# Optimization experiments

Hardware: AMD Instinct MI355X
Metric: run time of the kernel (lower is better)

The kernel has to match this reference:

```python
import jax, jax.numpy as jnp
import numpy as np

N = 16384   # total queries (= total keys here)
B = 16      # scenes
K = 1024    # keys per scene (key_batch_cnt entries)
L = 32      # local neighborhood size
D = 256     # d_model
H = 8       # nhead
DFF = 1024
LN_EPS = 1e-5


def setup_inputs() -> dict:
    key = jax.random.key(0)
    ks = jax.random.split(key, 32)
    f32 = jnp.float32

    def lin(k, o, i):
        return jax.random.normal(k, (o, i), f32) * 0.02

    idx = jax.random.randint(ks[3], (N, L), 0, K)
    invalid = jax.random.uniform(ks[4], (N, L)) < 0.1
    index_pair = jnp.where(invalid, -1, idx).astype(jnp.int32)

    inp = {
        "tgt": jax.random.normal(ks[0], (N, D), f32),
        "memory": jax.random.normal(ks[1], (N, D), f32),
        "memory_pos_emb": jax.random.normal(ks[2], (N, D), f32),
        "key_batch_cnt": jnp.full((B,), K, dtype=jnp.int32),
        "index_pair": index_pair,
        "index_pair_batch": jnp.repeat(jnp.arange(B, dtype=jnp.int32), K),
        "Wq": lin(ks[5], D, D), "bq": jnp.zeros((D,), f32),
        "Wkc": lin(ks[6], D, D), "bkc": jnp.zeros((D,), f32),
        "Wkp": lin(ks[7], D, D), "bkp": jnp.zeros((D,), f32),
        "Wv": lin(ks[8], D, D), "bv": jnp.zeros((D,), f32),
        "Wo": lin(ks[9], D, D), "bo": jnp.zeros((D,), f32),
        "W1": lin(ks[10], DFF, D), "b1": jnp.zeros((DFF,), f32),
        "W2": lin(ks[11], D, DFF), "b2": jnp.zeros((D,), f32),
        "g2": jnp.ones((D,), f32), "be2": jnp.zeros((D,), f32),
        "g3": jnp.ones((D,), f32), "be3": jnp.zeros((D,), f32),
    }
    return inp


def _ln(x, g, b):
    m = jnp.mean(x, axis=-1, keepdims=True)
    v = jnp.mean((x - m) ** 2, axis=-1, keepdims=True)
    return (x - m) * jax.lax.rsqrt(v + LN_EPS) * g + b


def reference(tgt, memory, memory_pos_emb, key_batch_cnt, index_pair,
              index_pair_batch, Wq, bq, Wkc, bkc, Wkp, bkp, Wv, bv,
              Wo, bo, W1, b1, W2, b2, g2, be2, g3, be3):
    Dh = D // H
    scale = Dh ** -0.5

    # dense projections
    q = tgt @ Wq.T + bq                              # [N, D]
    k = (memory @ Wkc.T + bkc) + (memory_pos_emb @ Wkp.T + bkp)  # content + pos
    v = memory @ Wv.T + bv

    # local-index gather: per-batch indices -> global key indices
    offsets = jnp.concatenate([jnp.zeros((1,), jnp.int32),
                               jnp.cumsum(key_batch_cnt)[:-1].astype(jnp.int32)])
    mask = index_pair < 0                            # [N, L] padded neighbors
    gidx = jnp.where(mask, 0, index_pair + offsets[index_pair_batch][:, None])

    kg = k[gidx].reshape(N, L, H, Dh)                # gathered keys  [N,L,H,Dh]
    vg = v[gidx].reshape(N, L, H, Dh)                # gathered values
    qh = q.reshape(N, H, Dh)

    attn = jnp.einsum('nhd,nlhd->nhl', qh, kg) * scale
    attn = jnp.where(mask[:, None, :], -1e9, attn)
    attn = jax.nn.softmax(attn, axis=-1)
    out = jnp.einsum('nhl,nlhd->nhd', attn, vg).reshape(N, D)
    tgt2 = out @ Wo.T + bo                           # attention out_proj

    x = _ln(tgt + tgt2, g2, be2)
    ff = jax.nn.relu(x @ W1.T + b1) @ W2.T + b2
    return _ln(x + ff, g3, be3)
```

## Files before the change

kernel.cpp:

```cpp
#include <hip/hip_runtime.h>
#include <stdint.h>

#define N_TOT 16384
#define LNEI  32
#define DM    256
#define NH    8
#define DH    32
#define DFF   1024

typedef __attribute__((ext_vector_type(8))) short  short8;
typedef __attribute__((ext_vector_type(4))) float  floatx4;
typedef __attribute__((ext_vector_type(4))) unsigned short ushort4_t;
typedef __attribute__((ext_vector_type(4))) unsigned int uint4_t;

static __device__ __forceinline__ float b2f(unsigned short u) {
  union { unsigned int u; float f; } x; x.u = ((unsigned int)u) << 16; return x.f;
}
static __device__ __forceinline__ unsigned short f2b(float f) {
  union { float f; unsigned int u; } x; x.f = f;
  unsigned int r = x.u + 0x7fffu + ((x.u >> 16) & 1u);
  return (unsigned short)(r >> 16);
}
static __device__ __forceinline__ float lo16(unsigned int d) {
  union { unsigned int u; float f; } x; x.u = d << 16; return x.f;
}
static __device__ __forceinline__ float hi16(unsigned int d) {
  union { unsigned int u; float f; } x; x.u = d & 0xffff0000u; return x.f;
}

#define NSEG 11
struct Seg { const float* src; unsigned short* dst; int cols; int ostride; int ooff; int begin; };
struct SegTable { Seg s[NSEG]; int total; };

__global__ __launch_bounds__(256) void cvt_all(SegTable T, float* biaskv,
                                               const float* bkc, const float* bkp,
                                               const float* bv) {
  int e = (blockIdx.x * 256 + threadIdx.x) * 4;
  if (e >= T.total) {
    int c = e - T.total;
    #pragma unroll
    for (int j = 0; j < 4; ++j, ++c)
      if (c < 512) biaskv[c] = (c < 256) ? (bkc[c] + bkp[c]) : bv[c - 256];
    return;
  }
  int si = 0;
  #pragma unroll
  for (int i = 1; i < NSEG; ++i) if (e >= T.s[i].begin) si = i;
  const Seg s = T.s[si];
  const int le = e - s.begin;
  const int row = le / s.cols;
  const int col = le - row * s.cols;
  floatx4 v = {0.f, 0.f, 0.f, 0.f};
  if (s.src) v = *(const floatx4*)(s.src + le);
  ushort4_t o;
  o.x = f2b(v[0]); o.y = f2b(v[1]); o.z = f2b(v[2]); o.w = f2b(v[3]);
  *(ushort4_t*)(s.dst + (size_t)row * s.ostride + s.ooff + col) = o;
}

static __device__ __forceinline__ void gl_lds16(const unsigned short* g, unsigned short* l) {
  __builtin_amdgcn_global_load_lds(
      (const __attribute__((address_space(1))) unsigned int*)g,
      (__attribute__((address_space(3))) unsigned int*)l, 16, 0, 0);
}

template<int BN, bool RELU>
__global__ __launch_bounds__(256) void gemm_tile(
    const unsigned short* __restrict__ A, const unsigned short* __restrict__ W,
    const float* __restrict__ bias,
    unsigned short* __restrict__ C, int M, int Nd, int K, int lda)
{
  constexpr int BM = 128, BK = 32;
  constexpr int MI = (BN == 128) ? 4 : 2;
  constexpr int NI = 4;
  __shared__ unsigned short sA[2][BM * BK];
  __shared__ unsigned short sB[2][BN * BK];

  const int w    = threadIdx.x >> 6;
  const int lane = threadIdx.x & 63;
  const int quad = lane >> 4;
  const int l16  = lane & 15;
  const int m0 = blockIdx.x * BM;
  const int n0 = blockIdx.y * BN;
  const int wrow0 = (BN == 128) ? (w >> 1) * 64 : w * 32;
  const int wcol0 = (BN == 128) ? (w & 1) * 64 : 0;

  const int aflat0 = w * 512 + lane * 8;
  const int ar0 = aflat0 >> 5, ac = aflat0 & 31;

  floatx4 acc[MI][NI] = {};

  for (int k0 = 0; k0 < K; k0 += 2 * BK) {
    __syncthreads();
    #pragma unroll
    for (int half = 0; half < 2; ++half) {
      const int kk = k0 + half * BK;
      #pragma unroll
      for (int c = 0; c < 2; ++c) {
        const int row = ar0 + c * 64;
        gl_lds16(A + (size_t)(m0 + row) * lda + kk + ac, &sA[half][(c * 4 + w) * 512]);
      }
      if (BN == 128) {
        #pragma unroll
        for (int c = 0; c < 2; ++c) {
          const int row = ar0 + c * 64;
          gl_lds16(W + (size_t)(n0 + row) * K + kk + ac, &sB[half][(c * 4 + w) * 512]);
        }
      } else {
        gl_lds16(W + (size_t)(n0 + ar0) * K + kk + ac, &sB[half][w * 512]);
      }
    }
    __syncthreads();

    #pragma unroll
    for (int half = 0; half < 2; ++half) {
      short8 af[MI], bf[NI];
      #pragma unroll
      for (int mi = 0; mi < MI; ++mi)
        af[mi] = *(const short8*)&sA[half][(wrow0 + mi * 16 + l16) * BK + quad * 8];
      #pragma unroll
      for (int ni = 0; ni < NI; ++ni)
        bf[ni] = *(const short8*)&sB[half][(wcol0 + ni * 16 + l16) * BK + quad * 8];
      #pragma unroll
      for (int mi = 0; mi < MI; ++mi)
        #pragma unroll
        for (int ni = 0; ni < NI; ++ni)
          acc[mi][ni] = __builtin_amdgcn_mfma_f32_16x16x32_bf16(af[mi], bf[ni], acc[mi][ni], 0, 0, 0);
    }
  }

  #pragma unroll
  for (int ni = 0; ni < NI; ++ni) {
    const int col = n0 + wcol0 + ni * 16 + l16;
    const float bvv = bias[col];
    #pragma unroll
    for (int mi = 0; mi < MI; ++mi) {
      const int row0 = m0 + wrow0 + mi * 16 + quad * 4;
      #pragma unroll
      for (int i = 0; i < 4; ++i) {
        float v = acc[mi][ni][i] + bvv;
        if (RELU) v = fmaxf(v, 0.f);
        C[(size_t)(row0 + i) * Nd + col] = f2b(v);
      }
    }
  }
}

__global__ __launch_bounds__(256) void attn_kernel(
    const unsigned short* __restrict__ q, const unsigned short* __restrict__ kv,
    const int* __restrict__ key_batch_cnt, const int* __restrict__ index_pair,
    const int* __restrict__ index_pair_batch,
    unsigned short* __restrict__ out)
{
  const int n = blockIdx.x;
  const int t = threadIdx.x;
  __shared__ float s_q[DM];
  __shared__ int   s_gidx[LNEI];
  __shared__ float s_prob[NH][LNEI];
  __shared__ float s_out[2][DM];

  s_q[t] = b2f(q[(size_t)n * DM + t]);
  if (t < LNEI) {
    const int b = index_pair_batch[n];
    int off = 0;
    for (int i = 0; i < b; ++i) off += key_batch_cnt[i];
    const int ip = index_pair[(size_t)n * LNEI + t];
    s_gidx[t] = (ip < 0) ? -1 : (ip + off);
  }
  __syncthreads();

  {
    const int h = t >> 5;
    const int l = t & 31;
    const int g = s_gidx[l];

    floatx4 qv[8];
    #pragma unroll
    for (int c = 0; c < 8; ++c) qv[c] = *(const floatx4*)&s_q[h * DH + c * 4];

    float score = -1e9f;
    if (g >= 0) {
      const uint4_t* kp = (const uint4_t*)(kv + (size_t)g * 512 + h * DH);
      float acc = 0.f;
      #pragma unroll
      for (int c = 0; c < 4; ++c) {
        uint4_t d = kp[c];
        acc += lo16(d.x) * qv[c * 2][0] + hi16(d.x) * qv[c * 2][1]
             + lo16(d.y) * qv[c * 2][2] + hi16(d.y) * qv[c * 2][3]
             + lo16(d.z) * qv[c * 2 + 1][0] + hi16(d.z) * qv[c * 2 + 1][1]
             + lo16(d.w) * qv[c * 2 + 1][2] + hi16(d.w) * qv[c * 2 + 1][3];
      }
      score = acc * 0.17677669529663687f;
    }

    float mx = score;
    #pragma unroll
    for (int msk = 16; msk >= 1; msk >>= 1) mx = fmaxf(mx, __shfl_xor(mx, msk, 64));
    const float e = __expf(score - mx);
    float sm = e;
    #pragma unroll
    for (int msk = 16; msk >= 1; msk >>= 1) sm += __shfl_xor(sm, msk, 64);
    s_prob[h][l] = e / sm;
  }
  __syncthreads();

  {
    const int jh  = t >> 7;
    const int h   = (t >> 4) & 7;
    const int dh2 = t & 15;
    float ax = 0.f, ay = 0.f;
    const unsigned short* vbase = kv + 256 + h * DH + dh2 * 2;
    #pragma unroll
    for (int j2 = 0; j2 < 16; ++j2) {
      const int j = jh * 16 + j2;
      int gj = s_gidx[j];
      gj = (gj < 0) ? 0 : gj;
      const float p = s_prob[h][j];
      const unsigned int d = *(const unsigned int*)(vbase + (size_t)gj * 512);
      ax += p * lo16(d);
      ay += p * hi16(d);
    }
    s_out[jh][h * DH + dh2 * 2]     = ax;
    s_out[jh][h * DH + dh2 * 2 + 1] = ay;
  }
  __syncthreads();

  out[(size_t)n * DM + t] = f2b(s_out[0][t] + s_out[1][t]);
}

template<bool IN1F32, bool OUTF32>
__global__ __launch_bounds__(256) void ln_kernel(
    const void* __restrict__ in1, const unsigned short* __restrict__ in2,
    const float* __restrict__ g, const float* __restrict__ b,
    void* __restrict__ out)
{
  const int n = blockIdx.x;
  const int t = threadIdx.x;
  const int wv = t >> 6;
  __shared__ float part[8];

  float a1;
  if (IN1F32) a1 = ((const float*)in1)[(size_t)n * DM + t];
  else        a1 = b2f(((const unsigned short*)in1)[(size_t)n * DM + t]);
  const float a = a1 + b2f(in2[(size_t)n * DM + t]);

  float s = a;
  #pragma unroll
  for (int msk = 32; msk >= 1; msk >>= 1) s += __shfl_xor(s, msk, 64);
  if ((t & 63) == 0) part[wv] = s;
  __syncthreads();
  const float mean = (part[0] + part[1] + part[2] + part[3]) * (1.0f / DM);
  const float d = a - mean;
  float s2 = d * d;
  #pragma unroll
  for (int msk = 32; msk >= 1; msk >>= 1) s2 += __shfl_xor(s2, msk, 64);
  if ((t & 63) == 0) part[4 + wv] = s2;
  __syncthreads();
  const float var = (part[4] + part[5] + part[6] + part[7]) * (1.0f / DM);
  const float y = d * rsqrtf(var + 1e-5f) * g[t] + b[t];
  if (OUTF32) ((float*)out)[(size_t)n * DM + t] = y;
  else        ((unsigned short*)out)[(size_t)n * DM + t] = f2b(y);
}

extern "C" void kernel_launch(void* const* d_in, const int* in_sizes, int n_in,
                              void* d_out, int out_size, void* d_ws, size_t ws_size,
                              hipStream_t stream) {
  const float* tgt  = (const float*)d_in[0];
  const float* mem  = (const float*)d_in[1];
  const float* pos  = (const float*)d_in[2];
  const int* kbc    = (const int*)d_in[3];
  const int* ipair  = (const int*)d_in[4];
  const int* ipb    = (const int*)d_in[5];
  const float* Wq   = (const float*)d_in[6];
  const float* bq   = (const float*)d_in[7];
  const float* Wkc  = (const float*)d_in[8];
  const float* bkc  = (const float*)d_in[9];
  const float* Wkp  = (const float*)d_in[10];
  const float* bkp  = (const float*)d_in[11];
  const float* Wv   = (const float*)d_in[12];
  const float* bvp  = (const float*)d_in[13];
  const float* Wo   = (const float*)d_in[14];
  const float* bo   = (const float*)d_in[15];
  const float* W1   = (const float*)d_in[16];
  const float* b1   = (const float*)d_in[17];
  const float* W2   = (const float*)d_in[18];
  const float* b2   = (const float*)d_in[19];
  const float* g2   = (const float*)d_in[20];
  const float* be2  = (const float*)d_in[21];
  const float* g3   = (const float*)d_in[22];
  const float* be3  = (const float*)d_in[23];

  const size_t NB = (size_t)N_TOT * DM;
  unsigned short* ws = (unsigned short*)d_ws;
  unsigned short* tgt_b = ws;
  unsigned short* ao_b  = ws;
  unsigned short* t2_b  = ws + NB;
  unsigned short* mp_b  = ws + 2 * NB;
  unsigned short* x_b   = ws + 2 * NB;
  unsigned short* ff_b  = ws + 3 * NB;
  unsigned short* q_b   = ws + 4 * NB;
  unsigned short* h1_b  = ws + 4 * NB;
  unsigned short* kv_b  = ws + 5 * NB;
  unsigned short* wgt   = ws + 8 * NB;
  unsigned short* Wq_b  = wgt;
  unsigned short* Wkv_b = wgt + 65536;
  unsigned short* Wo_b  = wgt + 65536 + 262144;
  unsigned short* W1_b  = wgt + 2 * 65536 + 262144;
  unsigned short* W2_b  = wgt + 2 * 65536 + 2 * 262144;
  float* bias_kv = (float*)(wgt + 2 * 65536 + 3 * 262144);

  SegTable T;
  int beg = 0, i = 0;
  auto seg = [&](const float* s, unsigned short* d, int cols, int ostride, int ooff, int nelem) {
    T.s[i].src = s; T.s[i].dst = d; T.s[i].cols = cols;
    T.s[i].ostride = ostride; T.s[i].ooff = ooff; T.s[i].begin = beg;
    beg += nelem; ++i;
  };
  seg(tgt, tgt_b, DM, DM, 0,   (int)NB);
  seg(mem, mp_b,  DM, 512, 0,  (int)NB);
  seg(pos, mp_b,  DM, 512, DM, (int)NB);
  seg(Wq,  Wq_b,  DM, DM, 0,   65536);
  seg(Wkc, Wkv_b, DM, 512, 0,  65536);
  seg(Wkp, Wkv_b, DM, 512, DM, 65536);
  seg(Wv,  Wkv_b + (size_t)256 * 512, DM, 512, 0, 65536);
  seg(nullptr, Wkv_b + (size_t)256 * 512, DM, 512, DM, 65536);
  seg(Wo,  Wo_b,  DM, DM, 0,   65536);
  seg(W1,  W1_b,  DM, DM, 0,   262144);
  seg(W2,  W2_b,  DFF, DFF, 0, 262144);
  T.total = beg;

  dim3 blk(256);
  cvt_all<<<dim3(T.total / 1024 + 1), blk, 0, stream>>>(T, bias_kv, bkc, bkp, bvp);

  dim3 gQ(N_TOT / 128, DM / 64);
  dim3 gKV(N_TOT / 128, 512 / 64);
  dim3 gF(N_TOT / 128, DFF / 128);

  gemm_tile<64, false><<<gQ, blk, 0, stream>>>(tgt_b, Wq_b, bq, q_b, N_TOT, DM, DM, DM);
  gemm_tile<64, false><<<gKV, blk, 0, stream>>>(mp_b, Wkv_b, bias_kv, kv_b, N_TOT, 512, 512, 512);
  attn_kernel<<<dim3(N_TOT), blk, 0, stream>>>(q_b, kv_b, kbc, ipair, ipb, ao_b);
  gemm_tile<64, false><<<gQ, blk, 0, stream>>>(ao_b, Wo_b, bo, t2_b, N_TOT, DM, DM, DM);
  ln_kernel<true, false><<<dim3(N_TOT), blk, 0, stream>>>(tgt, t2_b, g2, be2, x_b);
  gemm_tile<128, true><<<gF, blk, 0, stream>>>(x_b, W1_b, b1, h1_b, N_TOT, DFF, DM, DM);
  gemm_tile<64, false><<<gQ, blk, 0, stream>>>(h1_b, W2_b, b2, ff_b, N_TOT, DM, DFF, DFF);
  ln_kernel<false, true><<<dim3(N_TOT), blk, 0, stream>>>(x_b, ff_b, g3, be3, d_out);
}
```

Baseline: 278.6 us.

## Use single-wave 32x64 GEMM tiles for narrow projections and remap attention blocks

Adds a one-wavefront GEMM kernel with 32x64 output tiles and uses it for the Q, KV, out-proj and FFN-down projections. The goal is many more small workgroups, for better occupancy and load balance across CUs. Each tile now re-reads more weight data per output and runs on a single wave with no intra-block sharing. The attention kernel's block index is permuted to interleave queries across eight strided groups, which changes the order of key/value gathers for locality. The 128-wide GEMM template is simplified to handle only BN=128.

```diff
diff --git a/kernel.cpp b/kernel.cpp
--- a/kernel.cpp
+++ b/kernel.cpp
@@ -63,6 +63,75 @@
       (__attribute__((address_space(3))) unsigned int*)l, 16, 0, 0);
 }
 
+template<bool RELU>
+__global__ __launch_bounds__(64) void gemm_w1(
+    const unsigned short* __restrict__ A, const unsigned short* __restrict__ W,
+    const float* __restrict__ bias,
+    unsigned short* __restrict__ C, int M, int Nd, int K, int lda)
+{
+  constexpr int BK = 32;
+  __shared__ unsigned short sA[2][32 * BK];
+  __shared__ unsigned short sB[2][64 * BK];
+
+  const int lane = threadIdx.x;
+  const int quad = lane >> 4;
+  const int l16  = lane & 15;
+  const int m0 = blockIdx.x * 32;
+  const int n0 = blockIdx.y * 64;
+
+  const int srow = lane >> 2;
+  const int scol = (lane & 3) * 8;
+
+  floatx4 acc[2][4] = {};
+
+  for (int k0 = 0; k0 < K; k0 += 2 * BK) {
+    __syncthreads();
+    #pragma unroll
+    for (int half = 0; half < 2; ++half) {
+      const int kk = k0 + half * BK;
+      #pragma unroll
+      for (int c = 0; c < 2; ++c)
+        gl_lds16(A + (size_t)(m0 + c * 16 + srow) * lda + kk + scol, &sA[half][c * 512]);
+      #pragma unroll
+      for (int c = 0; c < 4; ++c)
+        gl_lds16(W + (size_t)(n0 + c * 16 + srow) * K + kk + scol, &sB[half][c * 512]);
+    }
+    __syncthreads();
+
+    #pragma unroll
+    for (int half = 0; half < 2; ++half) {
+      short8 af[2], bf[4];
+      #pragma unroll
+      for (int mi = 0; mi < 2; ++mi)
+        af[mi] = *(const short8*)&sA[half][(mi * 16 + l16) * BK + quad * 8];
+      #pragma unroll
+      for (int ni = 0; ni < 4; ++ni)
+        bf[ni] = *(const short8*)&sB[half][(ni * 16 + l16) * BK + quad * 8];
+      #pragma unroll
+      for (int mi = 0; mi < 2; ++mi)
+        #pragma unroll
+        for (int ni = 0; ni < 4; ++ni)
+          acc[mi][ni] = __builtin_amdgcn_mfma_f32_16x16x32_bf16(af[mi], bf[ni], acc[mi][ni], 0, 0, 0);
+    }
+  }
+
+  #pragma unroll
+  for (int ni = 0; ni < 4; ++ni) {
+    const int col = n0 + ni * 16 + l16;
+    const float bvv = bias[col];
+    #pragma unroll
+    for (int mi = 0; mi < 2; ++mi) {
+      const int row0 = m0 + mi * 16 + quad * 4;
+      #pragma unroll
+      for (int i = 0; i < 4; ++i) {
+        float v = acc[mi][ni][i] + bvv;
+        if (RELU) v = fmaxf(v, 0.f);
+        C[(size_t)(row0 + i) * Nd + col] = f2b(v);
+      }
+    }
+  }
+}
+
 template<int BN, bool RELU>
 __global__ __launch_bounds__(256) void gemm_tile(
     const unsigned short* __restrict__ A, const unsigned short* __restrict__ W,
@@ -70,8 +139,7 @@
     unsigned short* __restrict__ C, int M, int Nd, int K, int lda)
 {
   constexpr int BM = 128, BK = 32;
-  constexpr int MI = (BN == 128) ? 4 : 2;
-  constexpr int NI = 4;
+  constexpr int MI = 4, NI = 4;
   __shared__ unsigned short sA[2][BM * BK];
   __shared__ unsigned short sB[2][BN * BK];
 
@@ -81,8 +149,8 @@
   const int l16  = lane & 15;
   const int m0 = blockIdx.x * BM;
   const int n0 = blockIdx.y * BN;
-  const int wrow0 = (BN == 128) ? (w >> 1) * 64 : w * 32;
-  const int wcol0 = (BN == 128) ? (w & 1) * 64 : 0;
+  const int wrow0 = (w >> 1) * 64;
+  const int wcol0 = (w & 1) * 64;
 
   const int aflat0 = w * 512 + lane * 8;
   const int ar0 = aflat0 >> 5, ac = aflat0 & 31;
@@ -98,15 +166,7 @@
       for (int c = 0; c < 2; ++c) {
         const int row = ar0 + c * 64;
         gl_lds16(A + (size_t)(m0 + row) * lda + kk + ac, &sA[half][(c * 4 + w) * 512]);
-      }
-      if (BN == 128) {
-        #pragma unroll
-        for (int c = 0; c < 2; ++c) {
-          const int row = ar0 + c * 64;
-          gl_lds16(W + (size_t)(n0 + row) * K + kk + ac, &sB[half][(c * 4 + w) * 512]);
-        }
-      } else {
-        gl_lds16(W + (size_t)(n0 + ar0) * K + kk + ac, &sB[half][w * 512]);
+        gl_lds16(W + (size_t)(n0 + row) * K + kk + ac, &sB[half][(c * 4 + w) * 512]);
       }
     }
     __syncthreads();
@@ -151,7 +211,7 @@
     const int* __restrict__ index_pair_batch,
     unsigned short* __restrict__ out)
 {
-  const int n = blockIdx.x;
+  const int n = ((blockIdx.x & 7) << 11) | (blockIdx.x >> 3);
   const int t = threadIdx.x;
   __shared__ float s_q[DM];
   __shared__ int   s_gidx[LNEI];
@@ -331,16 +391,17 @@
   dim3 blk(256);
   cvt_all<<<dim3(T.total / 1024 + 1), blk, 0, stream>>>(T, bias_kv, bkc, bkp, bvp);
 
-  dim3 gQ(N_TOT / 128, DM / 64);
-  dim3 gKV(N_TOT / 128, 512 / 64);
+  dim3 blk64(64);
+  dim3 gQ(N_TOT / 32, DM / 64);
+  dim3 gKV(N_TOT / 32, 512 / 64);
   dim3 gF(N_TOT / 128, DFF / 128);
 
-  gemm_tile<64, false><<<gQ, blk, 0, stream>>>(tgt_b, Wq_b, bq, q_b, N_TOT, DM, DM, DM);
-  gemm_tile<64, false><<<gKV, blk, 0, stream>>>(mp_b, Wkv_b, bias_kv, kv_b, N_TOT, 512, 512, 512);
+  gemm_w1<false><<<gQ, blk64, 0, stream>>>(tgt_b, Wq_b, bq, q_b, N_TOT, DM, DM, DM);
+  gemm_w1<false><<<gKV, blk64, 0, stream>>>(mp_b, Wkv_b, bias_kv, kv_b, N_TOT, 512, 512, 512);
   attn_kernel<<<dim3(N_TOT), blk, 0, stream>>>(q_b, kv_b, kbc, ipair, ipb, ao_b);
-  gemm_tile<64, false><<<gQ, blk, 0, stream>>>(ao_b, Wo_b, bo, t2_b, N_TOT, DM, DM, DM);
+  gemm_w1<false><<<gQ, blk64, 0, stream>>>(ao_b, Wo_b, bo, t2_b, N_TOT, DM, DM, DM);
   ln_kernel<true, false><<<dim3(N_TOT), blk, 0, stream>>>(tgt, t2_b, g2, be2, x_b);
   gemm_tile<128, true><<<gF, blk, 0, stream>>>(x_b, W1_b, b1, h1_b, N_TOT, DFF, DM, DM);
-  gemm_tile<64, false><<<gQ, blk, 0, stream>>>(h1_b, W2_b, b2, ff_b, N_TOT, DM, DFF, DFF);
+  gemm_w1<false><<<gQ, blk64, 0, stream>>>(h1_b, W2_b, b2, ff_b, N_TOT, DM, DFF, DFF);
   ln_kernel<false, true><<<dim3(N_TOT), blk, 0, stream>>>(x_b, ff_b, g3, be3, d_out);
 }
```

New measurement: 291.9 us. +4.8%, slower.

## Coalesce key gather across neighbors and remap block order for XCD locality

Applied to the files above, without the earlier changes.

The QK score phase now assigns 8 threads to each neighbor, so every thread reads 16-byte chunks strided across the full 512-byte key row. The gathered key reads become contiguous per neighbor instead of one lane per neighbor per head. Partial dot products are reduced with shuffles and staged in a new shared score array, which costs an extra barrier before the softmax. Block indices are also permuted so that consecutive blocks, which are dispatched round-robin over the 8 XCDs, map to contiguous query ranges on each XCD. That keeps neighbors from the same scene in one XCD's L2.

```diff
diff --git a/kernel.cpp b/kernel.cpp
--- a/kernel.cpp
+++ b/kernel.cpp
@@ -151,10 +151,11 @@
     const int* __restrict__ index_pair_batch,
     unsigned short* __restrict__ out)
 {
-  const int n = blockIdx.x;
+  const int n = ((blockIdx.x & 7) << 11) | (blockIdx.x >> 3);
   const int t = threadIdx.x;
   __shared__ float s_q[DM];
   __shared__ int   s_gidx[LNEI];
+  __shared__ float s_score[NH][LNEI];
   __shared__ float s_prob[NH][LNEI];
   __shared__ float s_out[2][DM];
 
@@ -169,33 +170,46 @@
   __syncthreads();
 
   {
+    const int j  = t >> 3;
+    const int c8 = t & 7;
+    const int g  = s_gidx[j];
+    const int gl = (g < 0) ? 0 : g;
+    const unsigned short* kbase = kv + (size_t)gl * 512;
+
+    float part[4];
+    #pragma unroll
+    for (int i = 0; i < 4; ++i) {
+      const int c = c8 + i * 8;
+      const uint4_t d = *(const uint4_t*)(kbase + c * 8);
+      const float* qp = &s_q[c * 8];
+      part[i] = lo16(d.x) * qp[0] + hi16(d.x) * qp[1]
+              + lo16(d.y) * qp[2] + hi16(d.y) * qp[3]
+              + lo16(d.z) * qp[4] + hi16(d.z) * qp[5]
+              + lo16(d.w) * qp[6] + hi16(d.w) * qp[7];
+    }
+    #pragma unroll
+    for (int i = 0; i < 4; ++i) {
+      part[i] += __shfl_xor(part[i], 1, 64);
+      part[i] += __shfl_xor(part[i], 2, 64);
+    }
+    if ((c8 & 3) == 0) {
+      const int hodd = c8 >> 2;
+      #pragma unroll
+      for (int i = 0; i < 4; ++i)
+        s_score[2 * i + hodd][j] =
+            (g < 0) ? -1e9f : part[i] * 0.17677669529663687f;
+    }
+  }
+  __syncthreads();
+
+  {
     const int h = t >> 5;
     const int l = t & 31;
-    const int g = s_gidx[l];
-
-    floatx4 qv[8];
-    #pragma unroll
-    for (int c = 0; c < 8; ++c) qv[c] = *(const floatx4*)&s_q[h * DH + c * 4];
-
-    float score = -1e9f;
-    if (g >= 0) {
-      const uint4_t* kp = (const uint4_t*)(kv + (size_t)g * 512 + h * DH);
-      float acc = 0.f;
-      #pragma unroll
-      for (int c = 0; c < 4; ++c) {
-        uint4_t d = kp[c];
-        acc += lo16(d.x) * qv[c * 2][0] + hi16(d.x) * qv[c * 2][1]
-             + lo16(d.y) * qv[c * 2][2] + hi16(d.y) * qv[c * 2][3]
-             + lo16(d.z) * qv[c * 2 + 1][0] + hi16(d.z) * qv[c * 2 + 1][1]
-             + lo16(d.w) * qv[c * 2 + 1][2] + hi16(d.w) * qv[c * 2 + 1][3];
-      }
-      score = acc * 0.17677669529663687f;
-    }
-
-    float mx = score;
+    const float sc = s_score[h][l];
+    float mx = sc;
     #pragma unroll
     for (int msk = 16; msk >= 1; msk >>= 1) mx = fmaxf(mx, __shfl_xor(mx, msk, 64));
-    const float e = __expf(score - mx);
+    const float e = __expf(sc - mx);
     float sm = e;
     #pragma unroll
     for (int msk = 16; msk >= 1; msk >>= 1) sm += __shfl_xor(sm, msk, 64);
```

Result: no change. 273.4 us (-1.9%).
